# Optimization experiments

Measured on AMD Instinct MI355X. Metric: run time of the kernel, lower is better.

Reference implementation:

```python
import jax, jax.numpy as jnp
import numpy as np

B, N, NT, C, CO = 8, 12288, 3072, 256, 512
H0, W0 = 128, 96

def _grid_idx(loc, h, w):
    # loc in [-1,1] -> nearest grid cell index (matches token2map's round/clamp)
    loc = jnp.clip(jax.lax.stop_gradient(loc), -1.0, 1.0)
    xi = jnp.clip(jnp.round(0.5 * (loc[..., 0] + 1.0) * w - 0.5).astype(jnp.int32), 0, w - 1)
    yi = jnp.clip(jnp.round(0.5 * (loc[..., 1] + 1.0) * h - 0.5).astype(jnp.int32), 0, h - 1)
    return xi + yi * w

def _bn(x, gamma, beta):
    # BatchNorm (training-mode batch stats) over (B, N) per channel; x: (B, N, C)
    mean = x.mean(axis=(0, 1))
    var = ((x - mean) ** 2).mean(axis=(0, 1))
    return (x - mean) * jax.lax.rsqrt(var + 1e-5) * gamma + beta

def _token2map(x, loc, idx_agg, h, w):
    b, n, c = x.shape
    n0 = idx_agg.shape[1]
    seg = (_grid_idx(loc, h, w) + jnp.arange(b)[:, None] * (h * w)).reshape(-1)
    x_pt = jnp.take_along_axis(x, idx_agg[..., None], axis=1).reshape(b * n0, c)
    summed = jax.ops.segment_sum(x_pt, seg, num_segments=b * h * w)
    count = jax.ops.segment_sum(jnp.ones((b * n0,), x.dtype), seg, num_segments=b * h * w)
    x_map = summed / (count + 1e-6)[:, None]
    return x_map.reshape(b, h, w, c).transpose(0, 3, 1, 2)  # (B, C, H, W)

def _map2token(fmap, nt, loc, idx_agg_t, agg_weight_t):
    b, c, h, w = fmap.shape
    n0 = idx_agg_t.shape[1]
    idx_hw = _grid_idx(loc, h, w)
    fflat = fmap.reshape(b, c, h * w).transpose(0, 2, 1)  # (B, HW, C)
    feat = jnp.take_along_axis(fflat, idx_hw[..., None], axis=1)  # (B, N0, C)
    wgt = agg_weight_t.reshape(b, n0)
    seg = (idx_agg_t + jnp.arange(b)[:, None] * nt).reshape(-1)
    num = jax.ops.segment_sum((feat * wgt[..., None]).reshape(b * n0, c), seg, num_segments=b * nt)
    den = jax.ops.segment_sum(wgt.reshape(-1), seg, num_segments=b * nt) + 1e-6
    return (num / den[:, None]).reshape(b, nt, c)

def _token_downup(x_s, idx_agg_s, nt, idx_agg_t, agg_weight_t):
    b, s, c = x_s.shape
    n0 = idx_agg_s.shape[1]
    x_pt = jnp.take_along_axis(x_s, idx_agg_s[..., None], axis=1)  # (B, N0, C)
    wgt = agg_weight_t.reshape(b, n0)
    seg = (idx_agg_t + jnp.arange(b)[:, None] * nt).reshape(-1)
    num = jax.ops.segment_sum((x_pt * wgt[..., None]).reshape(b * n0, c), seg, num_segments=b * nt)
    den = jax.ops.segment_sum(wgt.reshape(-1), seg, num_segments=b * nt) + 1e-6
    return (num / den[:, None]).reshape(b, nt, c)

def setup_inputs():
    key = jax.random.key(0)
    ks = jax.random.split(key, 10)
    return {
        "x": jax.random.normal(ks[0], (B, N, C), jnp.float32),
        "loc_orig": jax.random.uniform(ks[1], (B, N, 2), jnp.float32, -1.0, 1.0),
        "idx_agg": jax.random.randint(ks[2], (B, N), 0, N),
        "agg_weight": jax.random.uniform(ks[3], (B, N, 1), jnp.float32),
        "x_t": jax.random.normal(ks[4], (B, NT, C), jnp.float32),
        "idx_agg_t": jax.random.randint(ks[5], (B, N), 0, NT),
        "agg_weight_t": jax.random.uniform(ks[6], (B, N, 1), jnp.float32),
        "H": H0, "W": W0,
        "dw_conv_w": jax.random.normal(ks[7], (C, 1, 3, 3), jnp.float32) * 0.1,
        "dw_skip_w": jax.random.normal(ks[8], (C, 1, 1, 1), jnp.float32) * 0.1,
        "norm1_gamma": jnp.ones((C,), jnp.float32),
        "norm1_beta": jnp.zeros((C,), jnp.float32),
        "conv_w": jax.random.normal(ks[9], (CO, C), jnp.float32) * (1.0 / np.sqrt(C)),
        "norm2_gamma": jnp.ones((CO,), jnp.float32),
        "norm2_beta": jnp.zeros((CO,), jnp.float32),
    }

def reference(x, loc_orig, idx_agg, agg_weight, x_t, idx_agg_t, agg_weight_t, H, W,
              dw_conv_w, dw_skip_w, norm1_gamma, norm1_beta, conv_w, norm2_gamma, norm2_beta):
    nt = x_t.shape[1]
    # token2map -> depthwise 3x3 stride-2 conv -> map2token (onto downsampled grid)
    x_map = _token2map(x, loc_orig, idx_agg, H, W)
    x_map = jax.lax.conv_general_dilated(
        x_map, dw_conv_w, window_strides=(2, 2), padding=((1, 1), (1, 1)),
        feature_group_count=x_map.shape[1],
        dimension_numbers=("NCHW", "OIHW", "NCHW"))
    x_map = _map2token(x_map, nt, loc_orig, idx_agg_t, agg_weight_t)
    # skip path: token_downup + 1x1 depthwise (per-channel scale)
    xd = _token_downup(x, idx_agg, nt, idx_agg_t, agg_weight_t)
    xd = xd * dw_skip_w.reshape(1, 1, -1)
    xd = xd + x_map
    xd = _bn(xd, norm1_gamma, norm1_beta)
    xd = jnp.einsum("bnc,oc->bno", xd, conv_w)  # 1x1 conv C -> CO
    xd = _bn(xd, norm2_gamma, norm2_beta)
    return jax.nn.relu(xd)
```

## Files before the change

### kernel.cpp

```cpp
#include <hip/hip_runtime.h>
#include <hip/hip_bf16.h>

using bf16 = __hip_bfloat16;
typedef __attribute__((ext_vector_type(8))) short bf16x8;
typedef __attribute__((ext_vector_type(4))) float f32x4;

#define BB   8
#define NN   12288
#define NTOK (BB*NN)
#define NTK  3072
#define CC   256
#define CCO  512
#define HH   128
#define WWI  96
#define HWIN (HH*WWI)
#define H2   64
#define W2   48
#define HW2  (H2*W2)
#define RR   (BB*NTK)

#define O_CONV  0LL
#define O_XD    6291456LL
#define O_AUX   9437184LL
#define O_WT    12582912LL
#define O_ST1   12713984LL
#define O_ST2   12714496LL
#define O_AB1   12715520LL
#define O_B2    12716032LL
#define O_AB2   12716544LL
#define O_FLAG  12717568LL
#define O_META  12717572LL
#define O_OFF   12914180LL
#define O_LIST  13037060LL

__device__ __forceinline__ float cvt(float v){ return v; }
__device__ __forceinline__ float cvt(bf16 v){ return __bfloat162float(v); }
template<typename T>
__device__ __forceinline__ float ld(const void* p, long long i){
    return cvt(((const T*)p)[i]);
}
__device__ __forceinline__ float bfu(unsigned short u){
    return __uint_as_float((unsigned)u << 16);
}
__device__ __forceinline__ unsigned short ubf(float f){
    bf16 h = __float2bfloat16(f);
    return *(unsigned short*)&h;
}
template<typename T>
__device__ __forceinline__ f32x4 ld4(const void* p, long long i);
template<>
__device__ __forceinline__ f32x4 ld4<bf16>(const void* p, long long i){
    const ushort4 u = *(const ushort4*)((const unsigned short*)p + i);
    return (f32x4){bfu(u.x), bfu(u.y), bfu(u.z), bfu(u.w)};
}
template<>
__device__ __forceinline__ f32x4 ld4<float>(const void* p, long long i){
    const float4 v = *(const float4*)((const float*)p + i);
    return (f32x4){v.x, v.y, v.z, v.w};
}

__global__ void k_flag(const float* __restrict__ locf, float* __restrict__ flag){
    if (threadIdx.x == 0){
        int bad = 0;
        for (int i = 0; i < 64; ++i){
            const float v = locf[i];
            if (!(v >= -1.0f && v <= 1.0f)) bad = 1;
        }
        flag[0] = bad ? 1.0f : 0.0f;
    }
}

__device__ __forceinline__ int2 gidx2(float lx, float ly, int h, int w){
    lx = fminf(fmaxf(lx, -1.f), 1.f);
    ly = fminf(fmaxf(ly, -1.f), 1.f);
    int xi = (int)rintf(0.5f*(lx+1.f)*(float)w - 0.5f);
    int yi = (int)rintf(0.5f*(ly+1.f)*(float)h - 0.5f);
    xi = min(max(xi,0), w-1); yi = min(max(yi,0), h-1);
    return make_int2(xi, yi);
}

template<typename T>
__device__ void meta_body(const void* loc, const int* __restrict__ iat, const void* wt,
                          int2* __restrict__ meta, int* __restrict__ off){
    const int tok = blockIdx.x*256 + threadIdx.x;
    const int b = tok / NN;
    const float lx = ld<T>(loc, 2LL*tok);
    const float ly = ld<T>(loc, 2LL*tok + 1);
    const int2 g1 = gidx2(lx, ly, HH, WWI);
    const int2 g2 = gidx2(lx, ly, H2, W2);
    const float wv = ld<T>(wt, tok);
    int2 m; m.x = g2.x + g2.y*W2; m.y = __float_as_int(wv);
    meta[tok] = m;
    atomicAdd(&off[b*HWIN + g1.x + g1.y*WWI], 1);
    atomicAdd(&off[NTOK + b*NTK + iat[tok]], 1);
}
__global__ __launch_bounds__(256) void k_meta(
        const void* loc, const int* __restrict__ iat, const void* wt,
        const float* __restrict__ flag, int2* __restrict__ meta,
        int* __restrict__ off){
    if (flag[0] != 0.0f) meta_body<bf16>(loc, iat, wt, meta, off);
    else                 meta_body<float>(loc, iat, wt, meta, off);
}

#define SCN  (NTOK + RR)
#define SCB  120
__global__ __launch_bounds__(1024) void k_scan1(int* __restrict__ off, int* __restrict__ aux){
    __shared__ int sm[1024];
    const int tid = threadIdx.x;
    const int gid = blockIdx.x*1024 + tid;
    const int v = off[gid];
    sm[tid] = v;
    __syncthreads();
    for (int d = 1; d < 1024; d <<= 1){
        const int t = (tid >= d) ? sm[tid-d] : 0;
        __syncthreads();
        sm[tid] += t;
        __syncthreads();
    }
    off[gid] = sm[tid] - v;
    if (tid == 1023) aux[blockIdx.x] = sm[1023];
}
__global__ __launch_bounds__(128) void k_scan2(int* __restrict__ aux){
    __shared__ int sm[128];
    const int tid = threadIdx.x;
    const int v = (tid < SCB) ? aux[tid] : 0;
    sm[tid] = v;
    __syncthreads();
    for (int d = 1; d < 128; d <<= 1){
        const int t = (tid >= d) ? sm[tid-d] : 0;
        __syncthreads();
        sm[tid] += t;
        __syncthreads();
    }
    if (tid < SCB) aux[tid] = sm[tid] - v;
}
__global__ __launch_bounds__(1024) void k_scan3(int* __restrict__ off, const int* __restrict__ aux){
    off[blockIdx.x*1024 + threadIdx.x] += aux[blockIdx.x];
}

template<typename T>
__device__ void fill_body(const void* loc, const int* __restrict__ ia,
                          const int* __restrict__ iat,
                          int* __restrict__ off, int* __restrict__ list){
    const int tok = blockIdx.x*256 + threadIdx.x;
    const int b = tok / NN;
    const float lx = ld<T>(loc, 2LL*tok);
    const float ly = ld<T>(loc, 2LL*tok + 1);
    const int2 g1 = gidx2(lx, ly, HH, WWI);
    const int pa = atomicAdd(&off[b*HWIN + g1.x + g1.y*WWI], 1);
    list[pa] = b*NN + ia[tok];
    const int pb = atomicAdd(&off[NTOK + b*NTK + iat[tok]], 1);
    list[pb] = tok;
}
__global__ __launch_bounds__(256) void k_fill(
        const void* loc, const int* __restrict__ ia, const int* __restrict__ iat,
        const float* __restrict__ flag,
        int* __restrict__ off, int* __restrict__ list){
    if (flag[0] != 0.0f) fill_body<bf16>(loc, ia, iat, off, list);
    else                 fill_body<float>(loc, ia, iat, off, list);
}

template<typename T>
__device__ void conv_body(const void* x, const void* dww,
                          const int* __restrict__ off, const int* __restrict__ list,
                          bf16* __restrict__ conv){
    const int wave = threadIdx.x >> 6;
    const int lane = threadIdx.x & 63;
    const int ch0 = lane*4;
    const int cell = blockIdx.x*4 + wave;
    const int b = cell / HW2;
    const int p = cell % HW2;
    const int oh = p / W2, ow = p % W2;

    f32x4 wreg[9];
    #pragma unroll
    for (int k = 0; k < 9; ++k)
        wreg[k] = (f32x4){ ld<T>(dww, (long long)(ch0  )*9 + k),
                           ld<T>(dww, (long long)(ch0+1)*9 + k),
                           ld<T>(dww, (long long)(ch0+2)*9 + k),
                           ld<T>(dww, (long long)(ch0+3)*9 + k) };

    const bool kw0v = (ow > 0);
    f32x4 acc = (f32x4){0.f,0.f,0.f,0.f};
    #pragma unroll
    for (int kh = 0; kh < 3; ++kh){
        const int ih = 2*oh - 1 + kh;
        if (ih < 0 || ih >= HH) continue;
        const int gbase = b*HWIN + ih*WWI + 2*ow - 1;
        const int e0 = (gbase >= 0) ? off[gbase] : 0;
        const int e1 = off[gbase+1];
        const int e2 = off[gbase+2];
        const int ms = kw0v ? off[gbase-1] : e0;
        f32x4 b0 = (f32x4){0.f,0.f,0.f,0.f};
        f32x4 b1 = (f32x4){0.f,0.f,0.f,0.f};
        f32x4 b2 = (f32x4){0.f,0.f,0.f,0.f};
        int idx = ms;
        while (idx < e2){
            const int cnt = min(e2 - idx, 64);
            const int tokv = (lane < cnt) ? list[idx + lane] : 0;
            for (int j = 0; j < cnt; ++j){
                const int row = __shfl(tokv, j);
                const f32x4 xv = ld4<T>(x, (long long)row*CC + ch0);
                const int gi = idx + j;
                if (gi < e0)      b0 += xv;
                else if (gi < e1) b1 += xv;
                else              b2 += xv;
            }
            idx += cnt;
        }
        const float r0 = 1.0f/((float)(e0 - ms) + 1e-6f);
        const float r1 = 1.0f/((float)(e1 - e0) + 1e-6f);
        const float r2 = 1.0f/((float)(e2 - e1) + 1e-6f);
        const f32x4 w0 = wreg[kh*3+0], w1 = wreg[kh*3+1], w2 = wreg[kh*3+2];
        #pragma unroll
        for (int c = 0; c < 4; ++c)
            acc[c] += w0[c]*b0[c]*r0 + w1[c]*b1[c]*r1 + w2[c]*b2[c]*r2;
    }
    ushort4 o;
    o.x = ubf(acc[0]); o.y = ubf(acc[1]); o.z = ubf(acc[2]); o.w = ubf(acc[3]);
    *(ushort4*)((unsigned short*)conv + (long long)cell*CC + ch0) = o;
}
__global__ __launch_bounds__(256) void k_conv(
        const void* x, const void* dww, const float* __restrict__ flag,
        const int* __restrict__ off, const int* __restrict__ list,
        bf16* __restrict__ conv){
    if (flag[0] != 0.0f) conv_body<bf16>(x, dww, off, list, conv);
    else                 conv_body<float>(x, dww, off, list, conv);
}

#define TGW 4
template<typename T>
__device__ void num_body(const void* x, const bf16* __restrict__ conv,
                         const void* skw, const int* __restrict__ ia,
                         const int2* __restrict__ meta,
                         const int* __restrict__ off, const int* __restrict__ list,
                         bf16* __restrict__ xdf, float* __restrict__ st1){
    __shared__ float ss[CC], sq[CC];
    const int tid = threadIdx.x;
    ss[tid] = 0.f; sq[tid] = 0.f;
    __syncthreads();
    const int wave = tid >> 6;
    const int lane = tid & 63;
    const int ch0 = lane*4;
    const f32x4 sk = ld4<T>(skw, ch0);
    float sa0=0.f,sa1=0.f,sa2=0.f,sa3=0.f, qa0=0.f,qa1=0.f,qa2=0.f,qa3=0.f;
    const int W = blockIdx.x*4 + wave;
    for (int t = 0; t < TGW; ++t){
        const int gt = W*TGW + t;
        const int b = gt / NTK;
        const int gj = NTOK + gt;
        const int e  = off[gj];
        const int s  = off[gj-1];
        f32x4 a = (f32x4){0.f,0.f,0.f,0.f};
        float den = 0.f;
        int idx = s;
        while (idx < e){
            const int cnt = min(e - idx, 64);
            int tok = 0, ja = 0; int2 m = make_int2(0, 0);
            if (lane < cnt){
                tok = list[idx + lane];
                m = meta[tok];
                ja = ia[tok];
            }
            for (int j = 0; j < cnt; ++j){
                const float wv = __int_as_float(__shfl(m.y, j));
                const int rx = b*NN  + __shfl(ja, j);
                const int rc = b*HW2 + __shfl(m.x, j);
                const f32x4 xv = ld4<T>(x, (long long)rx*CC + ch0);
                const f32x4 cv = ld4<bf16>(conv, (long long)rc*CC + ch0);
                #pragma unroll
                for (int c = 0; c < 4; ++c)
                    a[c] += wv*(sk[c]*xv[c] + cv[c]);
                den += wv;
            }
            idx += cnt;
        }
        const float rl = 1.0f/(den + 1e-6f);
        const float v0 = a[0]*rl, v1 = a[1]*rl, v2 = a[2]*rl, v3 = a[3]*rl;
        ushort4 o; o.x = ubf(v0); o.y = ubf(v1); o.z = ubf(v2); o.w = ubf(v3);
        const long long bi = (long long)(gt >> 4)*4096 + (long long)(ch0 >> 3)*128
                           + (long long)(gt & 15)*8 + (ch0 & 7);
        *(ushort4*)((unsigned short*)xdf + bi) = o;
        sa0 += v0; sa1 += v1; sa2 += v2; sa3 += v3;
        qa0 += v0*v0; qa1 += v1*v1; qa2 += v2*v2; qa3 += v3*v3;
    }
    atomicAdd(&ss[ch0  ], sa0); atomicAdd(&sq[ch0  ], qa0);
    atomicAdd(&ss[ch0+1], sa1); atomicAdd(&sq[ch0+1], qa1);
    atomicAdd(&ss[ch0+2], sa2); atomicAdd(&sq[ch0+2], qa2);
    atomicAdd(&ss[ch0+3], sa3); atomicAdd(&sq[ch0+3], qa3);
    __syncthreads();
    atomicAdd(&st1[tid], ss[tid]);
    atomicAdd(&st1[CC + tid], sq[tid]);
}
__global__ __launch_bounds__(256) void k_num(
        const void* x, const bf16* __restrict__ conv, const void* skw,
        const int* __restrict__ ia, const int2* __restrict__ meta,
        const int* __restrict__ off, const int* __restrict__ list,
        const float* __restrict__ flag,
        bf16* __restrict__ xdf, float* __restrict__ st1){
    if (flag[0] != 0.0f) num_body<bf16>(x, conv, skw, ia, meta, off, list, xdf, st1);
    else                 num_body<float>(x, conv, skw, ia, meta, off, list, xdf, st1);
}

template<typename T>
__device__ void bn1_body(const float* __restrict__ st1, const void* g1, const void* b1,
                         const void* cw, float* __restrict__ ab1, float* __restrict__ bias2){
    __shared__ float sb[CC];
    const int tid = threadIdx.x;
    if (tid < CC){
        const float mean = st1[tid]/(float)RR;
        const float var  = st1[CC + tid]/(float)RR - mean*mean;
        const float a  = ld<T>(g1, tid) * rsqrtf(var + 1e-5f);
        const float bb = ld<T>(b1, tid) - mean*a;
        ab1[tid] = a; ab1[CC + tid] = bb;
        sb[tid] = bb;
    }
    __syncthreads();
    float acc = 0.f;
    for (int c = 0; c < CC; ++c) acc += sb[c]*ld<T>(cw, (long long)tid*CC + c);
    bias2[tid] = acc;
}
__global__ __launch_bounds__(512) void k_bn1(
        const float* __restrict__ st1, const void* g1, const void* b1, const void* cw,
        const float* __restrict__ flag, float* __restrict__ ab1, float* __restrict__ bias2){
    if (flag[0] != 0.0f) bn1_body<bf16>(st1, g1, b1, cw, ab1, bias2);
    else                 bn1_body<float>(st1, g1, b1, cw, ab1, bias2);
}

template<typename T>
__device__ void wt_body(const void* cw, const float* __restrict__ ab1, bf16* __restrict__ wTf){
    const int c = blockIdx.x, o = threadIdx.x;
    const float v = ld<T>(cw, (long long)o*CC + c) * ab1[c];
    wTf[(((long long)(o >> 4)*32 + (c >> 3))*16 + (o & 15))*8 + (c & 7)] = __float2bfloat16(v);
}
__global__ __launch_bounds__(512) void k_wt(
        const void* cw, const float* __restrict__ ab1,
        const float* __restrict__ flag, bf16* __restrict__ wTf){
    if (flag[0] != 0.0f) wt_body<bf16>(cw, ab1, wTf);
    else                 wt_body<float>(cw, ab1, wTf);
}

__global__ __launch_bounds__(256) void k_gemm(
        const bf16* __restrict__ xdf, const bf16* __restrict__ wTf,
        const float* __restrict__ bias2, const float* __restrict__ flag,
        void* __restrict__ y, float* __restrict__ st2){
    __shared__ float ss[128], sq[128];
    const int tid = threadIdx.x;
    if (tid < 128){ ss[tid] = 0.f; sq[tid] = 0.f; }
    __syncthreads();
    const int wave = tid >> 6;
    const int lane = tid & 63;
    const int l16 = lane & 15;
    const int lq  = lane >> 4;
    const int mb = blockIdx.x;
    const int nb = blockIdx.y;
    const int mt = mb*4 + wave;
    const int n0t = nb*8;
    const short* ap = (const short*)xdf + ((long long)mt*32 + lq)*128 + (long long)l16*8;
    const short* bp = (const short*)wTf + ((long long)n0t*32 + lq)*128 + (long long)l16*8;
    f32x4 acc[8];
    #pragma unroll
    for (int nt = 0; nt < 8; ++nt) acc[nt] = (f32x4){0.f,0.f,0.f,0.f};
    #pragma unroll
    for (int kg0 = 0; kg0 < 8; ++kg0){
        const bf16x8 af = *((const bf16x8*)(ap + kg0*512));
        #pragma unroll
        for (int nt = 0; nt < 8; ++nt){
            const bf16x8 bfr = *((const bf16x8*)(bp + (long long)nt*4096 + kg0*512));
            acc[nt] = __builtin_amdgcn_mfma_f32_16x16x32_bf16(af, bfr, acc[nt], 0, 0, 0);
        }
    }
    const int row0 = mt*16 + lq*4;
    const bool isbf = (flag[0] != 0.0f);
    #pragma unroll
    for (int nt = 0; nt < 8; ++nt){
        const int col = nb*128 + nt*16 + l16;
        const float bz = bias2[col];
        float s = 0.f, q = 0.f;
        float v[4];
        #pragma unroll
        for (int r = 0; r < 4; ++r){
            v[r] = acc[nt][r] + bz;
            s += v[r]; q += v[r]*v[r];
        }
        if (isbf){
            bf16* yo = (bf16*)y;
            #pragma unroll
            for (int r = 0; r < 4; ++r)
                yo[(long long)(row0 + r)*CCO + col] = __float2bfloat16(v[r]);
        } else {
            float* yo = (float*)y;
            #pragma unroll
            for (int r = 0; r < 4; ++r)
                yo[(long long)(row0 + r)*CCO + col] = v[r];
        }
        s += __shfl_xor(s, 16); s += __shfl_xor(s, 32);
        q += __shfl_xor(q, 16); q += __shfl_xor(q, 32);
        if (lq == 0){
            atomicAdd(&ss[nt*16 + l16], s);
            atomicAdd(&sq[nt*16 + l16], q);
        }
    }
    __syncthreads();
    if (tid < 128){
        atomicAdd(&st2[nb*128 + tid], ss[tid]);
        atomicAdd(&st2[CCO + nb*128 + tid], sq[tid]);
    }
}

template<typename T>
__device__ void bn2_body(const float* __restrict__ st2, const void* g2, const void* b2,
                         float* __restrict__ ab2){
    const int tid = threadIdx.x;
    const float mean = st2[tid]/(float)RR;
    const float var  = st2[CCO + tid]/(float)RR - mean*mean;
    const float a = ld<T>(g2, tid) * rsqrtf(var + 1e-5f);
    ab2[tid] = a;
    ab2[CCO + tid] = ld<T>(b2, tid) - mean*a;
}
__global__ __launch_bounds__(512) void k_bn2(
        const float* __restrict__ st2, const void* g2, const void* b2,
        const float* __restrict__ flag, float* __restrict__ ab2){
    if (flag[0] != 0.0f) bn2_body<bf16>(st2, g2, b2, ab2);
    else                 bn2_body<float>(st2, g2, b2, ab2);
}

__global__ __launch_bounds__(256) void k_out(
        void* __restrict__ y, const float* __restrict__ ab2,
        const float* __restrict__ flag){
    const long long i0 = ((long long)blockIdx.x*256 + threadIdx.x)*4;
    const int o0 = (int)(i0 & (CCO-1));
    if (flag[0] != 0.0f){
        unsigned short* p = (unsigned short*)y;
        ushort4 u = *(ushort4*)(p + i0);
        float v0 = bfu(u.x)*ab2[o0  ] + ab2[CCO + o0  ];
        float v1 = bfu(u.y)*ab2[o0+1] + ab2[CCO + o0+1];
        float v2 = bfu(u.z)*ab2[o0+2] + ab2[CCO + o0+2];
        float v3 = bfu(u.w)*ab2[o0+3] + ab2[CCO + o0+3];
        u.x = ubf(fmaxf(v0,0.f)); u.y = ubf(fmaxf(v1,0.f));
        u.z = ubf(fmaxf(v2,0.f)); u.w = ubf(fmaxf(v3,0.f));
        *(ushort4*)(p + i0) = u;
    } else {
        float* p = (float*)y;
        float4 v = *(float4*)(p + i0);
        v.x = fmaxf(v.x*ab2[o0  ] + ab2[CCO + o0  ], 0.f);
        v.y = fmaxf(v.y*ab2[o0+1] + ab2[CCO + o0+1], 0.f);
        v.z = fmaxf(v.z*ab2[o0+2] + ab2[CCO + o0+2], 0.f);
        v.w = fmaxf(v.w*ab2[o0+3] + ab2[CCO + o0+3], 0.f);
        *(float4*)(p + i0) = v;
    }
}

extern "C" void kernel_launch(void* const* d_in, const int* in_sizes, int n_in,
                              void* d_out, int out_size, void* d_ws, size_t ws_size,
                              hipStream_t stream){
    (void)in_sizes; (void)n_in; (void)out_size; (void)ws_size;
    const void* x   = d_in[0];
    const void* loc = d_in[1];
    const int*  ia  = (const int*)d_in[2];
    const int*  iat = (const int*)d_in[5];
    const void* wt  = d_in[6];
    const void* dww = d_in[9];
    const void* skw = d_in[10];
    const void* g1  = d_in[11];
    const void* b1  = d_in[12];
    const void* cw  = d_in[13];
    const void* g2  = d_in[14];
    const void* b2  = d_in[15];
    float* ws = (float*)d_ws;
    float* flag = ws + O_FLAG;
    int*  off  = (int*)(ws + O_OFF);
    int*  list = (int*)(ws + O_LIST);
    int*  aux  = (int*)(ws + O_AUX);
    int2* meta = (int2*)(ws + O_META);
    bf16* conv = (bf16*)(ws + O_CONV);
    bf16* xdf  = (bf16*)(ws + O_XD);
    bf16* wTf  = (bf16*)(ws + O_WT);

    hipMemsetAsync(ws + O_ST1, 0, (size_t)1536*4, stream);
    hipMemsetAsync(off, 0, (size_t)SCN*4, stream);

    k_flag<<<dim3(1), dim3(64), 0, stream>>>((const float*)loc, flag);

    k_meta<<<dim3(NTOK/256), dim3(256), 0, stream>>>(loc, iat, wt, flag, meta, off);

    k_scan1<<<dim3(SCB), dim3(1024), 0, stream>>>(off, aux);
    k_scan2<<<dim3(1), dim3(128), 0, stream>>>(aux);
    k_scan3<<<dim3(SCB), dim3(1024), 0, stream>>>(off, aux);

    k_fill<<<dim3(NTOK/256), dim3(256), 0, stream>>>(loc, ia, iat, flag, off, list);

    k_conv<<<dim3(BB*HW2/4), dim3(256), 0, stream>>>(x, dww, flag, off, list, conv);

    k_num<<<dim3(RR/(4*TGW)), dim3(256), 0, stream>>>(
        x, conv, skw, ia, meta, off, list, flag, xdf, ws + O_ST1);

    k_bn1<<<dim3(1), dim3(512), 0, stream>>>(
        ws + O_ST1, g1, b1, cw, flag, ws + O_AB1, ws + O_B2);

    k_wt<<<dim3(CC), dim3(512), 0, stream>>>(cw, ws + O_AB1, flag, wTf);

    k_gemm<<<dim3(384, 4), dim3(256), 0, stream>>>(
        xdf, wTf, ws + O_B2, flag, d_out, ws + O_ST2);

    k_bn2<<<dim3(1), dim3(512), 0, stream>>>(ws + O_ST2, g2, b2, flag, ws + O_AB2);

    k_out<<<dim3((RR*CCO)/1024, 1), dim3(256), 0, stream>>>(d_out, ws + O_AB2, flag);
}
```

Measured before the change: 409.0 us.

## Split conv kernel rows across waves, unroll gathers, merge num token pairs, fold bias into wt

The depthwise conv now gives each output cell its own block and one wave per kernel row, reducing the three row partials through shared memory. Gather loops in conv and num are unrolled by four so several independent loads are in flight at once. The num kernel handles two adjacent target tokens per wave in one merged pass over their contiguous list range. The bias2 matvec moves out of the single-block bn1 kernel into k_wt via atomics, which relies on the enlarged memset to zero bias2 and adds many atomics.

```diff
diff --git a/kernel.cpp b/kernel.cpp
--- a/kernel.cpp
+++ b/kernel.cpp
@@ -164,33 +164,30 @@
 __device__ void conv_body(const void* x, const void* dww,
                           const int* __restrict__ off, const int* __restrict__ list,
                           bf16* __restrict__ conv){
-    const int wave = threadIdx.x >> 6;
-    const int lane = threadIdx.x & 63;
+    __shared__ f32x4 red[3][64];
+    const int tid = threadIdx.x;
+    const int kh = tid >> 6;
+    const int lane = tid & 63;
     const int ch0 = lane*4;
-    const int cell = blockIdx.x*4 + wave;
+    const int cell = blockIdx.x;
     const int b = cell / HW2;
     const int p = cell % HW2;
     const int oh = p / W2, ow = p % W2;
-
-    f32x4 wreg[9];
-    #pragma unroll
-    for (int k = 0; k < 9; ++k)
-        wreg[k] = (f32x4){ ld<T>(dww, (long long)(ch0  )*9 + k),
-                           ld<T>(dww, (long long)(ch0+1)*9 + k),
-                           ld<T>(dww, (long long)(ch0+2)*9 + k),
-                           ld<T>(dww, (long long)(ch0+3)*9 + k) };
-
-    const bool kw0v = (ow > 0);
-    f32x4 acc = (f32x4){0.f,0.f,0.f,0.f};
-    #pragma unroll
-    for (int kh = 0; kh < 3; ++kh){
-        const int ih = 2*oh - 1 + kh;
-        if (ih < 0 || ih >= HH) continue;
+    const int ih = 2*oh - 1 + kh;
+    f32x4 part = (f32x4){0.f,0.f,0.f,0.f};
+    if (ih >= 0){
         const int gbase = b*HWIN + ih*WWI + 2*ow - 1;
         const int e0 = (gbase >= 0) ? off[gbase] : 0;
         const int e1 = off[gbase+1];
         const int e2 = off[gbase+2];
-        const int ms = kw0v ? off[gbase-1] : e0;
+        const int ms = (ow > 0) ? off[gbase-1] : e0;
+        f32x4 w0, w1, w2;
+        #pragma unroll
+        for (int c = 0; c < 4; ++c){
+            w0[c] = ld<T>(dww, (long long)(ch0+c)*9 + kh*3 + 0);
+            w1[c] = ld<T>(dww, (long long)(ch0+c)*9 + kh*3 + 1);
+            w2[c] = ld<T>(dww, (long long)(ch0+c)*9 + kh*3 + 2);
+        }
         f32x4 b0 = (f32x4){0.f,0.f,0.f,0.f};
         f32x4 b1 = (f32x4){0.f,0.f,0.f,0.f};
         f32x4 b2 = (f32x4){0.f,0.f,0.f,0.f};
@@ -198,9 +195,25 @@
         while (idx < e2){
             const int cnt = min(e2 - idx, 64);
             const int tokv = (lane < cnt) ? list[idx + lane] : 0;
-            for (int j = 0; j < cnt; ++j){
-                const int row = __shfl(tokv, j);
-                const f32x4 xv = ld4<T>(x, (long long)row*CC + ch0);
+            int j = 0;
+            for (; j + 4 <= cnt; j += 4){
+                int oxs[4];
+                #pragma unroll
+                for (int u = 0; u < 4; ++u)
+                    oxs[u] = __shfl(tokv, j+u)*CC + ch0;
+                f32x4 xv[4];
+                #pragma unroll
+                for (int u = 0; u < 4; ++u) xv[u] = ld4<T>(x, (long long)oxs[u]);
+                #pragma unroll
+                for (int u = 0; u < 4; ++u){
+                    const int gi = idx + j + u;
+                    if (gi < e0)      b0 += xv[u];
+                    else if (gi < e1) b1 += xv[u];
+                    else              b2 += xv[u];
+                }
+            }
+            for (; j < cnt; ++j){
+                const f32x4 xv = ld4<T>(x, (long long)(__shfl(tokv, j)*CC + ch0));
                 const int gi = idx + j;
                 if (gi < e0)      b0 += xv;
                 else if (gi < e1) b1 += xv;
@@ -211,16 +224,25 @@
         const float r0 = 1.0f/((float)(e0 - ms) + 1e-6f);
         const float r1 = 1.0f/((float)(e1 - e0) + 1e-6f);
         const float r2 = 1.0f/((float)(e2 - e1) + 1e-6f);
-        const f32x4 w0 = wreg[kh*3+0], w1 = wreg[kh*3+1], w2 = wreg[kh*3+2];
         #pragma unroll
         for (int c = 0; c < 4; ++c)
-            acc[c] += w0[c]*b0[c]*r0 + w1[c]*b1[c]*r1 + w2[c]*b2[c]*r2;
-    }
-    ushort4 o;
-    o.x = ubf(acc[0]); o.y = ubf(acc[1]); o.z = ubf(acc[2]); o.w = ubf(acc[3]);
-    *(ushort4*)((unsigned short*)conv + (long long)cell*CC + ch0) = o;
-}
-__global__ __launch_bounds__(256) void k_conv(
+            part[c] = w0[c]*b0[c]*r0 + w1[c]*b1[c]*r1 + w2[c]*b2[c]*r2;
+    }
+    red[kh][lane] = part;
+    __syncthreads();
+    if (kh == 0){
+        const f32x4 t0 = red[0][lane];
+        const f32x4 t1 = red[1][lane];
+        const f32x4 t2 = red[2][lane];
+        ushort4 o;
+        o.x = ubf(t0[0]+t1[0]+t2[0]);
+        o.y = ubf(t0[1]+t1[1]+t2[1]);
+        o.z = ubf(t0[2]+t1[2]+t2[2]);
+        o.w = ubf(t0[3]+t1[3]+t2[3]);
+        *(ushort4*)((unsigned short*)conv + (long long)cell*CC + ch0) = o;
+    }
+}
+__global__ __launch_bounds__(192) void k_conv(
         const void* x, const void* dww, const float* __restrict__ flag,
         const int* __restrict__ off, const int* __restrict__ list,
         bf16* __restrict__ conv){
@@ -228,7 +250,7 @@
     else                 conv_body<float>(x, dww, off, list, conv);
 }
 
-#define TGW 4
+#define TGW 2
 template<typename T>
 __device__ void num_body(const void* x, const bf16* __restrict__ conv,
                          const void* skw, const int* __restrict__ ia,
@@ -243,39 +265,70 @@
     const int lane = tid & 63;
     const int ch0 = lane*4;
     const f32x4 sk = ld4<T>(skw, ch0);
+    const int W = blockIdx.x*4 + wave;
+    const int gt0 = W*TGW;
+    const int b = gt0 / NTK;
+    int offv = 0;
+    if (lane <= TGW) offv = off[NTOK + gt0 - 1 + lane];
+    const int s0  = __shfl(offv, 0);
+    const int eb0 = __shfl(offv, 1);
+    const int eb1 = __shfl(offv, 2);
+    f32x4 a0 = (f32x4){0.f,0.f,0.f,0.f};
+    f32x4 a1 = (f32x4){0.f,0.f,0.f,0.f};
+    float d0 = 0.f, d1 = 0.f;
+    int idx = s0;
+    while (idx < eb1){
+        const int cnt = min(eb1 - idx, 64);
+        int tok = 0, ja = 0; int2 m = make_int2(0, 0);
+        if (lane < cnt){
+            tok = list[idx + lane];
+            m = meta[tok];
+            ja = ia[tok];
+        }
+        int j = 0;
+        for (; j + 4 <= cnt; j += 4){
+            float wv[4]; int ox[4], oc[4];
+            #pragma unroll
+            for (int u = 0; u < 4; ++u){
+                wv[u] = __int_as_float(__shfl(m.y, j+u));
+                ox[u] = (b*NN  + __shfl(ja,  j+u))*CC + ch0;
+                oc[u] = (b*HW2 + __shfl(m.x, j+u))*CC + ch0;
+            }
+            f32x4 xv[4], cv[4];
+            #pragma unroll
+            for (int u = 0; u < 4; ++u) xv[u] = ld4<T>(x, (long long)ox[u]);
+            #pragma unroll
+            for (int u = 0; u < 4; ++u) cv[u] = ld4<bf16>(conv, (long long)oc[u]);
+            #pragma unroll
+            for (int u = 0; u < 4; ++u){
+                f32x4 cb;
+                #pragma unroll
+                for (int c = 0; c < 4; ++c) cb[c] = wv[u]*(sk[c]*xv[u][c] + cv[u][c]);
+                if (idx + j + u < eb0){ a0 += cb; d0 += wv[u]; }
+                else                  { a1 += cb; d1 += wv[u]; }
+            }
+        }
+        for (; j < cnt; ++j){
+            const float wv = __int_as_float(__shfl(m.y, j));
+            const int ox = (b*NN  + __shfl(ja,  j))*CC + ch0;
+            const int oc = (b*HW2 + __shfl(m.x, j))*CC + ch0;
+            const f32x4 xv = ld4<T>(x, (long long)ox);
+            const f32x4 cv = ld4<bf16>(conv, (long long)oc);
+            f32x4 cb;
+            #pragma unroll
+            for (int c = 0; c < 4; ++c) cb[c] = wv*(sk[c]*xv[c] + cv[c]);
+            if (idx + j < eb0){ a0 += cb; d0 += wv; }
+            else              { a1 += cb; d1 += wv; }
+        }
+        idx += cnt;
+    }
     float sa0=0.f,sa1=0.f,sa2=0.f,sa3=0.f, qa0=0.f,qa1=0.f,qa2=0.f,qa3=0.f;
-    const int W = blockIdx.x*4 + wave;
+    #pragma unroll
     for (int t = 0; t < TGW; ++t){
-        const int gt = W*TGW + t;
-        const int b = gt / NTK;
-        const int gj = NTOK + gt;
-        const int e  = off[gj];
-        const int s  = off[gj-1];
-        f32x4 a = (f32x4){0.f,0.f,0.f,0.f};
-        float den = 0.f;
-        int idx = s;
-        while (idx < e){
-            const int cnt = min(e - idx, 64);
-            int tok = 0, ja = 0; int2 m = make_int2(0, 0);
-            if (lane < cnt){
-                tok = list[idx + lane];
-                m = meta[tok];
-                ja = ia[tok];
-            }
-            for (int j = 0; j < cnt; ++j){
-                const float wv = __int_as_float(__shfl(m.y, j));
-                const int rx = b*NN  + __shfl(ja, j);
-                const int rc = b*HW2 + __shfl(m.x, j);
-                const f32x4 xv = ld4<T>(x, (long long)rx*CC + ch0);
-                const f32x4 cv = ld4<bf16>(conv, (long long)rc*CC + ch0);
-                #pragma unroll
-                for (int c = 0; c < 4; ++c)
-                    a[c] += wv*(sk[c]*xv[c] + cv[c]);
-                den += wv;
-            }
-            idx += cnt;
-        }
-        const float rl = 1.0f/(den + 1e-6f);
+        const f32x4 a  = (t == 0) ? a0 : a1;
+        const float dn = (t == 0) ? d0 : d1;
+        const int gt = gt0 + t;
+        const float rl = 1.0f/(dn + 1e-6f);
         const float v0 = a[0]*rl, v1 = a[1]*rl, v2 = a[2]*rl, v3 = a[3]*rl;
         ushort4 o; o.x = ubf(v0); o.y = ubf(v1); o.z = ubf(v2); o.w = ubf(v3);
         const long long bi = (long long)(gt >> 4)*4096 + (long long)(ch0 >> 3)*128
@@ -304,40 +357,36 @@
 
 template<typename T>
 __device__ void bn1_body(const float* __restrict__ st1, const void* g1, const void* b1,
-                         const void* cw, float* __restrict__ ab1, float* __restrict__ bias2){
-    __shared__ float sb[CC];
-    const int tid = threadIdx.x;
-    if (tid < CC){
-        const float mean = st1[tid]/(float)RR;
-        const float var  = st1[CC + tid]/(float)RR - mean*mean;
-        const float a  = ld<T>(g1, tid) * rsqrtf(var + 1e-5f);
-        const float bb = ld<T>(b1, tid) - mean*a;
-        ab1[tid] = a; ab1[CC + tid] = bb;
-        sb[tid] = bb;
-    }
-    __syncthreads();
-    float acc = 0.f;
-    for (int c = 0; c < CC; ++c) acc += sb[c]*ld<T>(cw, (long long)tid*CC + c);
-    bias2[tid] = acc;
-}
-__global__ __launch_bounds__(512) void k_bn1(
-        const float* __restrict__ st1, const void* g1, const void* b1, const void* cw,
-        const float* __restrict__ flag, float* __restrict__ ab1, float* __restrict__ bias2){
-    if (flag[0] != 0.0f) bn1_body<bf16>(st1, g1, b1, cw, ab1, bias2);
-    else                 bn1_body<float>(st1, g1, b1, cw, ab1, bias2);
-}
-
-template<typename T>
-__device__ void wt_body(const void* cw, const float* __restrict__ ab1, bf16* __restrict__ wTf){
+                         float* __restrict__ ab1){
+    const int tid = threadIdx.x;
+    const float mean = st1[tid]/(float)RR;
+    const float var  = st1[CC + tid]/(float)RR - mean*mean;
+    const float a  = ld<T>(g1, tid) * rsqrtf(var + 1e-5f);
+    ab1[tid] = a;
+    ab1[CC + tid] = ld<T>(b1, tid) - mean*a;
+}
+__global__ __launch_bounds__(256) void k_bn1(
+        const float* __restrict__ st1, const void* g1, const void* b1,
+        const float* __restrict__ flag, float* __restrict__ ab1){
+    if (flag[0] != 0.0f) bn1_body<bf16>(st1, g1, b1, ab1);
+    else                 bn1_body<float>(st1, g1, b1, ab1);
+}
+
+template<typename T>
+__device__ void wt_body(const void* cw, const float* __restrict__ ab1,
+                        bf16* __restrict__ wTf, float* __restrict__ bias2){
     const int c = blockIdx.x, o = threadIdx.x;
-    const float v = ld<T>(cw, (long long)o*CC + c) * ab1[c];
-    wTf[(((long long)(o >> 4)*32 + (c >> 3))*16 + (o & 15))*8 + (c & 7)] = __float2bfloat16(v);
+    const float w = ld<T>(cw, (long long)o*CC + c);
+    wTf[(((long long)(o >> 4)*32 + (c >> 3))*16 + (o & 15))*8 + (c & 7)] =
+        __float2bfloat16(w * ab1[c]);
+    atomicAdd(&bias2[o], w * ab1[CC + c]);
 }
 __global__ __launch_bounds__(512) void k_wt(
         const void* cw, const float* __restrict__ ab1,
-        const float* __restrict__ flag, bf16* __restrict__ wTf){
-    if (flag[0] != 0.0f) wt_body<bf16>(cw, ab1, wTf);
-    else                 wt_body<float>(cw, ab1, wTf);
+        const float* __restrict__ flag, bf16* __restrict__ wTf,
+        float* __restrict__ bias2){
+    if (flag[0] != 0.0f) wt_body<bf16>(cw, ab1, wTf, bias2);
+    else                 wt_body<float>(cw, ab1, wTf, bias2);
 }
 
 __global__ __launch_bounds__(256) void k_gemm(
@@ -477,7 +526,7 @@
     bf16* xdf  = (bf16*)(ws + O_XD);
     bf16* wTf  = (bf16*)(ws + O_WT);
 
-    hipMemsetAsync(ws + O_ST1, 0, (size_t)1536*4, stream);
+    hipMemsetAsync(ws + O_ST1, 0, (size_t)2560*4, stream);
     hipMemsetAsync(off, 0, (size_t)SCN*4, stream);
 
     k_flag<<<dim3(1), dim3(64), 0, stream>>>((const float*)loc, flag);
@@ -490,15 +539,15 @@
 
     k_fill<<<dim3(NTOK/256), dim3(256), 0, stream>>>(loc, ia, iat, flag, off, list);
 
-    k_conv<<<dim3(BB*HW2/4), dim3(256), 0, stream>>>(x, dww, flag, off, list, conv);
+    k_conv<<<dim3(BB*HW2), dim3(192), 0, stream>>>(x, dww, flag, off, list, conv);
 
     k_num<<<dim3(RR/(4*TGW)), dim3(256), 0, stream>>>(
         x, conv, skw, ia, meta, off, list, flag, xdf, ws + O_ST1);
 
-    k_bn1<<<dim3(1), dim3(512), 0, stream>>>(
-        ws + O_ST1, g1, b1, cw, flag, ws + O_AB1, ws + O_B2);
-
-    k_wt<<<dim3(CC), dim3(512), 0, stream>>>(cw, ws + O_AB1, flag, wTf);
+    k_bn1<<<dim3(1), dim3(256), 0, stream>>>(
+        ws + O_ST1, g1, b1, flag, ws + O_AB1);
+
+    k_wt<<<dim3(CC), dim3(512), 0, stream>>>(cw, ws + O_AB1, flag, wTf, ws + O_B2);
 
     k_gemm<<<dim3(384, 4), dim3(256), 0, stream>>>(
         xdf, wTf, ws + O_B2, flag, d_out, ws + O_ST2);
```

Measured after the change: 405.0 us. About the same (-1.0%).
